# Kernel optimization log

Hardware: AMD Instinct MI355X
Metric: run time of the kernel (lower is better)

The kernel has to match this reference:

```python
import jax, jax.numpy as jnp
import numpy as np

N_CAM, C, H, W = 4, 336, 96, 176
D, HB, WB = 6, 240, 120

def setup_inputs() -> dict:
    key = jax.random.key(0)
    k1, k2, k3, k4, k5 = jax.random.split(key, 5)
    return {
        "input": jax.random.normal(k1, (N_CAM, C, H, W), dtype=jnp.float32),
        "projection_u": jax.random.randint(k2, (N_CAM, D, HB, WB), 0, W, dtype=jnp.int32),
        "projection_v": jax.random.randint(k3, (N_CAM, D, HB, WB), 0, H, dtype=jnp.int32),
        "projection_valid": jax.random.randint(k4, (N_CAM, D, HB, WB), 0, 2, dtype=jnp.int32),
        "projection_density": jax.random.uniform(k5, (N_CAM, D, HB, WB), dtype=jnp.float32),
    }

def reference(input, projection_u, projection_v, projection_valid, projection_density):
    """Project2Dto3D: per-voxel gather from each camera feature map at (v,u),
    masked by validity and weighted by density normalization, summed over cameras.
    Output layout: [1, D*C, HB, WB] (336*6 = 2016 channels)."""
    def gather_cam(feat, u, v, valid, dens):
        # feat: (C,H,W); u,v,valid,dens: (D,HB,WB)
        g = feat[:, v, u]                                   # (C,D,HB,WB) gather
        w = valid.astype(feat.dtype) * dens                 # (D,HB,WB)
        return g * w[None]
    per_cam = jax.vmap(gather_cam)(input, projection_u, projection_v,
                                   projection_valid, projection_density)  # (N,C,D,HB,WB)
    out = per_cam.sum(axis=0)                               # (C,D,HB,WB)
    out = jnp.transpose(out, (1, 0, 2, 3))                  # (D,C,HB,WB)
    return out.reshape(1, D * C, HB, WB)
```

## Files before the change

### kernel.cpp

```cpp
#include <hip/hip_runtime.h>

#define NCAM 4
#define C 336
#define H 96
#define W 176
#define D 6
#define HB 240
#define WB 120
#define HW (H * W)
#define WBPB 60
#define NWP 2

static __device__ __forceinline__ unsigned short f2bf(float f) {
    unsigned u = __float_as_uint(f);
    unsigned r = (u + 0x7fffu + ((u >> 16) & 1u)) >> 16;
    return (unsigned short)r;
}

__global__ __launch_bounds__(256)
void vp_transpose_bf16(const float* __restrict__ in,
                       unsigned short* __restrict__ out) {
    __shared__ float tile[64][33];
    const int cam = blockIdx.z;
    const int hw0 = blockIdx.x * 64;
    const int c0  = blockIdx.y * 32;
    const int tid = threadIdx.x;

    const int hwq = tid & 15;
    const int cl  = tid >> 4;
    const float* src = in + (size_t)cam * C * HW + hw0 + hwq * 4;
#pragma unroll
    for (int cc = 0; cc < 2; ++cc) {
        const int c = c0 + cl + cc * 16;
        if (c < C) {
            const float4 v = *(const float4*)(src + (size_t)c * HW);
            tile[hwq * 4 + 0][cl + cc * 16] = v.x;
            tile[hwq * 4 + 1][cl + cc * 16] = v.y;
            tile[hwq * 4 + 2][cl + cc * 16] = v.z;
            tile[hwq * 4 + 3][cl + cc * 16] = v.w;
        }
    }
    __syncthreads();

    const int hw  = tid >> 2;
    const int oct = tid & 3;
    const int cs  = c0 + oct * 8;
    if (cs < C) {
        uint4 r;
        unsigned* pr = (unsigned*)&r;
#pragma unroll
        for (int k = 0; k < 4; ++k) {
            unsigned lo = f2bf(tile[hw][oct * 8 + 2 * k]);
            unsigned hi = f2bf(tile[hw][oct * 8 + 2 * k + 1]);
            pr[k] = lo | (hi << 16);
        }
        *(uint4*)(out + (size_t)cam * HW * C + (size_t)(hw0 + hw) * C + cs) = r;
    }
}

__global__ __launch_bounds__(256, 8)
void vp_gather_bf16(const unsigned short* __restrict__ tfeat,
                    const int* __restrict__ pu, const int* __restrict__ pv,
                    const int* __restrict__ pvalid,
                    const float* __restrict__ pdens,
                    float* __restrict__ out) {
    __shared__ int   s_off[NCAM][WBPB];
    __shared__ float s_wgt[NCAM][WBPB];
    __shared__ float s_acc[56][61];

    const int d   = blockIdx.x / HB;
    const int hb  = blockIdx.x % HB;
    const int wb0 = blockIdx.y * WBPB;
    const int tid = threadIdx.x;

    if (tid < NCAM * WBPB) {
        const int cam = tid / WBPB, wbl = tid % WBPB;
        const size_t pidx = ((size_t)(cam * D + d) * HB + hb) * WB + wb0 + wbl;
        s_wgt[cam][wbl] = pvalid[pidx] ? pdens[pidx] : 0.0f;
        s_off[cam][wbl] = cam * (HW * C) + (pv[pidx] * W + pu[pidx]) * C;
    }
    __syncthreads();

    const int wave  = tid >> 6;
    const int lane  = tid & 63;
    const int cq    = lane & 15;
    const int wbsub = lane >> 4;
    const bool cact = (cq < 14);
    const int coff  = (cact ? cq : 13) * 8;

    int wbc[4];
#pragma unroll
    for (int wbi = 0; wbi < 4; ++wbi) {
        const int wbl = wbsub + 4 * wbi;
        wbc[wbi] = wave * 15 + (wbl < 15 ? wbl : 14);
    }

#pragma unroll
    for (int cp = 0; cp < 3; ++cp) {
        float acc[4][8];
#pragma unroll
        for (int i = 0; i < 4; ++i)
#pragma unroll
            for (int j = 0; j < 8; ++j) acc[i][j] = 0.0f;

#pragma unroll
        for (int cam = 0; cam < NCAM; ++cam) {
            uint4 q[4];
#pragma unroll
            for (int wbi = 0; wbi < 4; ++wbi)
                q[wbi] = *(const uint4*)(tfeat +
                    (unsigned)(s_off[cam][wbc[wbi]] + coff + cp * 112));
#pragma unroll
            for (int wbi = 0; wbi < 4; ++wbi) {
                const float w = s_wgt[cam][wbc[wbi]];
                const uint4 v = q[wbi];
                acc[wbi][0] += w * __uint_as_float(v.x << 16);
                acc[wbi][1] += w * __uint_as_float(v.x & 0xffff0000u);
                acc[wbi][2] += w * __uint_as_float(v.y << 16);
                acc[wbi][3] += w * __uint_as_float(v.y & 0xffff0000u);
                acc[wbi][4] += w * __uint_as_float(v.z << 16);
                acc[wbi][5] += w * __uint_as_float(v.z & 0xffff0000u);
                acc[wbi][6] += w * __uint_as_float(v.w << 16);
                acc[wbi][7] += w * __uint_as_float(v.w & 0xffff0000u);
            }
        }

#pragma unroll
        for (int half = 0; half < 2; ++half) {
            if (cact && cq >= half * 7 && cq < half * 7 + 7) {
                const int rbase = (cq - half * 7) * 8;
#pragma unroll
                for (int wbi = 0; wbi < 4; ++wbi) {
                    const int wbl = wbsub + 4 * wbi;
                    if (wbl < 15) {
#pragma unroll
                        for (int j = 0; j < 8; ++j)
                            s_acc[rbase + j][wave * 15 + wbl] = acc[wbi][j];
                    }
                }
            }
            __syncthreads();

            const int wp = tid & 31;
            const int rb = tid >> 5;
            if (wp < 30) {
#pragma unroll
                for (int k = 0; k < 7; ++k) {
                    const int r = rb + 8 * k;
                    const int c = cp * 112 + half * 56 + r;
                    float2 v;
                    v.x = s_acc[r][wp * 2 + 0];
                    v.y = s_acc[r][wp * 2 + 1];
                    *(float2*)(out + (((size_t)d * C + c) * HB + hb) * WB +
                               wb0 + wp * 2) = v;
                }
            }
            __syncthreads();
        }
    }
}

extern "C" void kernel_launch(void* const* d_in, const int* in_sizes, int n_in,
                              void* d_out, int out_size, void* d_ws,
                              size_t ws_size, hipStream_t stream) {
    const float* feat  = (const float*)d_in[0];
    const int* pu      = (const int*)d_in[1];
    const int* pv      = (const int*)d_in[2];
    const int* pvalid  = (const int*)d_in[3];
    const float* pdens = (const float*)d_in[4];
    float* out         = (float*)d_out;

    unsigned short* tfeat = (unsigned short*)d_ws;

    dim3 tgrid(HW / 64, (C + 31) / 32, NCAM);
    vp_transpose_bf16<<<tgrid, 256, 0, stream>>>(feat, tfeat);

    dim3 ggrid(D * HB, NWP);
    vp_gather_bf16<<<ggrid, 256, 0, stream>>>(tfeat, pu, pv, pvalid, pdens,
                                              out);
}
```

Before: 201.6 us.

## Software-pipeline gather loads with inline asm and merge WB halves into one block

Each gather block now covers the full WB row with 512 threads instead of two 256-thread blocks. Feature loads are issued through inline asm global_load_dwordx4, and the next channel group's 16 loads are in flight while the previous group's accumulators are staged through LDS and stored. Manual vmcnt waits and sched_barriers keep that order fixed. This targets gather latency and barrier stalls, at the cost of more registers (q[4][4], voff), lower occupancy limits (launch_bounds 512,2) and fragile hand-written waitcnt counting.

```diff
diff --git a/kernel.cpp b/kernel.cpp
--- a/kernel.cpp
+++ b/kernel.cpp
@@ -8,8 +8,8 @@
 #define HB 240
 #define WB 120
 #define HW (H * W)
-#define WBPB 60
-#define NWP 2
+
+typedef unsigned u32x4 __attribute__((ext_vector_type(4)));
 
 static __device__ __forceinline__ unsigned short f2bf(float f) {
     unsigned u = __float_as_uint(f);
@@ -58,26 +58,68 @@
     }
 }
 
-__global__ __launch_bounds__(256, 8)
+#define LOADQ(dst, off, TF) \
+    asm volatile("global_load_dwordx4 %0, %1, %2" \
+                 : "=v"(dst) : "v"(off), "s"(TF))
+
+#define VMWAIT(N) \
+    do { asm volatile("s_waitcnt vmcnt(" #N ")" ::: "memory"); \
+         __builtin_amdgcn_sched_barrier(0); } while (0)
+
+#define LBAR() \
+    do { asm volatile("s_waitcnt lgkmcnt(0)" ::: "memory"); \
+         __builtin_amdgcn_sched_barrier(0); \
+         __builtin_amdgcn_s_barrier(); } while (0)
+
+#define ISSUE16() \
+    do { \
+        _Pragma("unroll") \
+        for (int cam = 0; cam < 4; ++cam) { \
+            _Pragma("unroll") \
+            for (int wbi = 0; wbi < 4; ++wbi) { \
+                LOADQ(q[cam][wbi], voff[cam][wbi], tfeat); \
+                voff[cam][wbi] += 224u; \
+            } \
+        } \
+    } while (0)
+
+#define FMACAM(cam, NW, OP) \
+    do { \
+        VMWAIT(NW); \
+        _Pragma("unroll") \
+        for (int wbi = 0; wbi < 4; ++wbi) { \
+            const float w = s_wgt[cam][wbc[wbi]]; \
+            const u32x4 v = q[cam][wbi]; \
+            acc[wbi][0] OP w * __uint_as_float(v[0] << 16); \
+            acc[wbi][1] OP w * __uint_as_float(v[0] & 0xffff0000u); \
+            acc[wbi][2] OP w * __uint_as_float(v[1] << 16); \
+            acc[wbi][3] OP w * __uint_as_float(v[1] & 0xffff0000u); \
+            acc[wbi][4] OP w * __uint_as_float(v[2] << 16); \
+            acc[wbi][5] OP w * __uint_as_float(v[2] & 0xffff0000u); \
+            acc[wbi][6] OP w * __uint_as_float(v[3] << 16); \
+            acc[wbi][7] OP w * __uint_as_float(v[3] & 0xffff0000u); \
+        } \
+    } while (0)
+
+__global__ __launch_bounds__(512, 2)
 void vp_gather_bf16(const unsigned short* __restrict__ tfeat,
                     const int* __restrict__ pu, const int* __restrict__ pv,
                     const int* __restrict__ pvalid,
                     const float* __restrict__ pdens,
                     float* __restrict__ out) {
-    __shared__ int   s_off[NCAM][WBPB];
-    __shared__ float s_wgt[NCAM][WBPB];
-    __shared__ float s_acc[56][61];
+    __shared__ int   s_off[NCAM][WB];
+    __shared__ float s_wgt[NCAM][WB];
+    __shared__ float s_acc[56][121];
 
     const int d   = blockIdx.x / HB;
     const int hb  = blockIdx.x % HB;
-    const int wb0 = blockIdx.y * WBPB;
     const int tid = threadIdx.x;
 
-    if (tid < NCAM * WBPB) {
-        const int cam = tid / WBPB, wbl = tid % WBPB;
-        const size_t pidx = ((size_t)(cam * D + d) * HB + hb) * WB + wb0 + wbl;
-        s_wgt[cam][wbl] = pvalid[pidx] ? pdens[pidx] : 0.0f;
-        s_off[cam][wbl] = cam * (HW * C) + (pv[pidx] * W + pu[pidx]) * C;
+    if (tid < NCAM * WB) {
+        const int cam = tid / WB, wb = tid % WB;
+        const size_t pidx = ((size_t)(cam * D + d) * HB + hb) * WB + wb;
+        s_wgt[cam][wb] = pvalid[pidx] ? pdens[pidx] : 0.0f;
+        s_off[cam][wb] = cam * (HW * C) + (pv[pidx] * W + pu[pidx]) * C;
     }
     __syncthreads();
 
@@ -95,36 +137,17 @@
         wbc[wbi] = wave * 15 + (wbl < 15 ? wbl : 14);
     }
 
-#pragma unroll
-    for (int cp = 0; cp < 3; ++cp) {
-        float acc[4][8];
-#pragma unroll
-        for (int i = 0; i < 4; ++i)
-#pragma unroll
-            for (int j = 0; j < 8; ++j) acc[i][j] = 0.0f;
-
-#pragma unroll
-        for (int cam = 0; cam < NCAM; ++cam) {
-            uint4 q[4];
-#pragma unroll
-            for (int wbi = 0; wbi < 4; ++wbi)
-                q[wbi] = *(const uint4*)(tfeat +
-                    (unsigned)(s_off[cam][wbc[wbi]] + coff + cp * 112));
-#pragma unroll
-            for (int wbi = 0; wbi < 4; ++wbi) {
-                const float w = s_wgt[cam][wbc[wbi]];
-                const uint4 v = q[wbi];
-                acc[wbi][0] += w * __uint_as_float(v.x << 16);
-                acc[wbi][1] += w * __uint_as_float(v.x & 0xffff0000u);
-                acc[wbi][2] += w * __uint_as_float(v.y << 16);
-                acc[wbi][3] += w * __uint_as_float(v.y & 0xffff0000u);
-                acc[wbi][4] += w * __uint_as_float(v.z << 16);
-                acc[wbi][5] += w * __uint_as_float(v.z & 0xffff0000u);
-                acc[wbi][6] += w * __uint_as_float(v.w << 16);
-                acc[wbi][7] += w * __uint_as_float(v.w & 0xffff0000u);
-            }
-        }
-
+    unsigned voff[4][4];
+#pragma unroll
+    for (int cam = 0; cam < 4; ++cam)
+#pragma unroll
+        for (int wbi = 0; wbi < 4; ++wbi)
+            voff[cam][wbi] = (unsigned)(s_off[cam][wbc[wbi]] + coff) * 2u;
+
+    u32x4 q[4][4];
+    float acc[4][8];
+
+    auto dumpstore = [&](int cp) {
 #pragma unroll
         for (int half = 0; half < 2; ++half) {
             if (cact && cq >= half * 7 && cq < half * 7 + 7) {
@@ -139,11 +162,10 @@
                     }
                 }
             }
-            __syncthreads();
-
-            const int wp = tid & 31;
-            const int rb = tid >> 5;
-            if (wp < 30) {
+            LBAR();
+            const int wp = tid & 63;
+            const int rb = tid >> 6;
+            if (wp < 60) {
 #pragma unroll
                 for (int k = 0; k < 7; ++k) {
                     const int r = rb + 8 * k;
@@ -152,12 +174,31 @@
                     v.x = s_acc[r][wp * 2 + 0];
                     v.y = s_acc[r][wp * 2 + 1];
                     *(float2*)(out + (((size_t)d * C + c) * HB + hb) * WB +
-                               wb0 + wp * 2) = v;
+                               wp * 2) = v;
                 }
             }
-            __syncthreads();
+            LBAR();
         }
-    }
+    };
+
+    ISSUE16();
+    FMACAM(0, 12, =);
+    FMACAM(1, 8, +=);
+    FMACAM(2, 4, +=);
+    FMACAM(3, 0, +=);
+    ISSUE16();
+    dumpstore(0);
+    FMACAM(0, 26, =);
+    FMACAM(1, 22, +=);
+    FMACAM(2, 18, +=);
+    FMACAM(3, 14, +=);
+    ISSUE16();
+    dumpstore(1);
+    FMACAM(0, 26, =);
+    FMACAM(1, 22, +=);
+    FMACAM(2, 18, +=);
+    FMACAM(3, 14, +=);
+    dumpstore(2);
 }
 
 extern "C" void kernel_launch(void* const* d_in, const int* in_sizes, int n_in,
@@ -175,7 +216,6 @@
     dim3 tgrid(HW / 64, (C + 31) / 32, NCAM);
     vp_transpose_bf16<<<tgrid, 256, 0, stream>>>(feat, tfeat);
 
-    dim3 ggrid(D * HB, NWP);
-    vp_gather_bf16<<<ggrid, 256, 0, stream>>>(tfeat, pu, pv, pvalid, pdens,
-                                              out);
-}
+    vp_gather_bf16<<<D * HB, 512, 0, stream>>>(tfeat, pu, pv, pvalid, pdens,
+                                               out);
+}
```

Result: faster. 175.1 us (-13.1%).
